# Optimization experiments

Hardware: AMD Instinct MI355X
Metric: run time of the kernel (lower is better)

The kernel has to match this reference:

```python
import jax, jax.numpy as jnp
import numpy as np

HEADS = 8
DIM_HEAD = 64
QUERY_DIM = 1024
CONTEXT_DIM = 768
INNER = HEADS * DIM_HEAD  # 512


def setup_inputs() -> dict:
    key = jax.random.key(0)
    ks = jax.random.split(key, 7)
    B, Sq, Skv = 4, 4096, 1024
    x = jax.random.normal(ks[0], (B, Sq, QUERY_DIM), dtype=jnp.float32)
    context = jax.random.normal(ks[1], (B, Skv, CONTEXT_DIM), dtype=jnp.float32)
    # nn.Linear(in, out) weights stored as [out, in]; we use [in, out] for x @ W
    Wq = jax.random.normal(ks[2], (QUERY_DIM, INNER), dtype=jnp.float32) * (QUERY_DIM ** -0.5)
    Wk = jax.random.normal(ks[3], (CONTEXT_DIM, INNER), dtype=jnp.float32) * (CONTEXT_DIM ** -0.5)
    Wv = jax.random.normal(ks[4], (CONTEXT_DIM, INNER), dtype=jnp.float32) * (CONTEXT_DIM ** -0.5)
    Wo = jax.random.normal(ks[5], (INNER, QUERY_DIM), dtype=jnp.float32) * (INNER ** -0.5)
    bo = jax.random.normal(ks[6], (QUERY_DIM,), dtype=jnp.float32) * 0.01
    return {"x": x, "context": context, "Wq": Wq, "Wk": Wk, "Wv": Wv, "Wo": Wo, "bo": bo}


def reference(x, context, Wq, Wk, Wv, Wo, bo):
    B, Sq, _ = x.shape
    h, d = HEADS, DIM_HEAD
    scale = d ** -0.5
    # project and split heads: [B, S, h*d] -> [B, h, S, d]
    q = (x @ Wq).reshape(B, Sq, h, d).transpose(0, 2, 1, 3)
    k = (context @ Wk).reshape(B, -1, h, d).transpose(0, 2, 1, 3)
    v = (context @ Wv).reshape(B, -1, h, d).transpose(0, 2, 1, 3)
    # the torch chunked loop is exactly full softmax attention (softmax is row-wise)
    scores = jnp.einsum('bhid,bhjd->bhij', q, k) * scale
    attn = jax.nn.softmax(scores, axis=-1)
    out = jnp.einsum('bhij,bhjd->bhid', attn, v)  # [B, h, Sq, d]
    out = out.transpose(0, 2, 1, 3).reshape(B, Sq, h * d)
    return out @ Wo + bo
```

## Files before the change

kernel.cpp:

```cpp
#include <hip/hip_runtime.h>

#define SQ 4096
#define SKV 1024
#define BATCH 4
#define NH 8
#define DH 64
#define QD 1024
#define CD 768
#define INNER 512

typedef _Float16 half8 __attribute__((ext_vector_type(8)));
typedef _Float16 half4v __attribute__((ext_vector_type(4)));
typedef float floatx4 __attribute__((ext_vector_type(4)));
typedef float f32x16 __attribute__((ext_vector_type(16)));
typedef unsigned int uint4v __attribute__((ext_vector_type(4)));

#define MFMA16(a, b, c) __builtin_amdgcn_mfma_f32_16x16x32_f16(a, b, c, 0, 0, 0)
#define MFMA32(a, b, c) __builtin_amdgcn_mfma_f32_32x32x16_f16(a, b, c, 0, 0, 0)

#define PLSWAP(a, b) asm("v_permlane32_swap_b32 %0, %1" : "+v"(a), "+v"(b))

#define GLD16(gptr, lptr)                                                            \
  __builtin_amdgcn_global_load_lds(                                                  \
      (const __attribute__((address_space(1))) unsigned int*)(const void*)(gptr),    \
      (__attribute__((address_space(3))) unsigned int*)(void*)(lptr), 16, 0, 0)

__global__ __launch_bounds__(256) void prep(const float* __restrict__ x,
                                            const float* __restrict__ ctx,
                                            const float* __restrict__ Wq,
                                            const float* __restrict__ Wk,
                                            const float* __restrict__ Wv,
                                            const float* __restrict__ Wo,
                                            _Float16* __restrict__ xh,
                                            _Float16* __restrict__ ctxh,
                                            _Float16* __restrict__ wqt,
                                            _Float16* __restrict__ wkvt,
                                            _Float16* __restrict__ wot) {
  __shared__ float tile[32][33];
  const size_t NX = (size_t)BATCH * SQ * QD;
  const size_t NC = (size_t)BATCH * SKV * CD;
  const unsigned NCAST = (unsigned)((NX + NC) / 2048);

  if (blockIdx.x < NCAST) {
    size_t i = ((size_t)blockIdx.x * 256 + threadIdx.x) * 8;
    const float* s;
    _Float16* d;
    size_t off;
    if (i < NX) { s = x; d = xh; off = i; }
    else        { s = ctx; d = ctxh; off = i - NX; }
    floatx4 a = *(const floatx4*)(s + off);
    floatx4 b = *(const floatx4*)(s + off + 4);
    half8 h;
#pragma unroll
    for (int j = 0; j < 4; ++j) { h[j] = (_Float16)a[j]; h[4 + j] = (_Float16)b[j]; }
    *(half8*)(d + off) = h;
    return;
  }
  const unsigned t = blockIdx.x - NCAST;
  const int z = t >> 10, rem = t & 1023;
  const float* src; _Float16* dst; int R, C;
  if (z == 0)      { src = Wq; dst = wqt;                        R = QD;    C = INNER; }
  else if (z == 1) { src = Wk; dst = wkvt;                       R = CD;    C = INNER; }
  else if (z == 2) { src = Wv; dst = wkvt + (size_t)INNER * CD;  R = CD;    C = INNER; }
  else             { src = Wo; dst = wot;                        R = INNER; C = QD;   }
  const int c0 = (rem & 31) * 32, r0 = (rem >> 5) * 32;
  if (c0 >= C || r0 >= R) return;
  const int tx = threadIdx.x & 31, ty = threadIdx.x >> 5;
#pragma unroll
  for (int i = 0; i < 32; i += 8)
    tile[ty + i][tx] = src[(size_t)(r0 + ty + i) * C + c0 + tx];
  __syncthreads();
#pragma unroll
  for (int i = 0; i < 32; i += 8)
    dst[(size_t)(c0 + ty + i) * R + r0 + tx] = (_Float16)tile[tx][ty + i];
}

template <int MODE>
__device__ __forceinline__ void gemm_body(const _Float16* __restrict__ A,
                                          const _Float16* __restrict__ Bt,
                                          void* __restrict__ Cout,
                                          void* __restrict__ Cout2,
                                          const float* __restrict__ bias,
                                          int M, int N, int K, int bx, int by,
                                          _Float16* As16, _Float16* Bs) {
  const int tid = threadIdx.x;
  const int wave = tid >> 6, lane = tid & 63;
  const int quad = lane >> 4, l16 = lane & 15;
  const int wm = (wave >> 1) * 64, wn = (wave & 1) * 64;
  const size_t n0 = (size_t)bx * 128, m0 = (size_t)by * 128;

  floatx4 acc[4][4] = {};

  const _Float16* ag = A + (m0 + (tid >> 2)) * (size_t)K + (tid & 3) * 8;
  const _Float16* bg = Bt + (n0 + (tid >> 2)) * (size_t)K + (tid & 3) * 8;

#define GSTAGE(bi, k0)                                                      \
  do {                                                                      \
    GLD16(ag + (k0), As16 + (bi)*4096 + tid * 8);                           \
    GLD16(ag + (k0) + (size_t)64 * K, As16 + (bi)*4096 + tid * 8 + 2048);   \
    GLD16(bg + (k0), Bs + (bi)*4096 + tid * 8);                             \
    GLD16(bg + (k0) + (size_t)64 * K, Bs + (bi)*4096 + tid * 8 + 2048);     \
  } while (0)

  const int NT = K / 32;
  GSTAGE(0, 0);
  for (int t = 0; t < NT; ++t) {
    __syncthreads();
    if (t + 1 < NT) GSTAGE((t + 1) & 1, (t + 1) * 32);
    const _Float16* as = As16 + (t & 1) * 4096;
    const _Float16* bs = Bs + (t & 1) * 4096;

    half8 af[4], bf[4];
#pragma unroll
    for (int mt = 0; mt < 4; ++mt)
      af[mt] = *(const half8*)(as + (wm + mt * 16 + l16) * 32 + quad * 8);
#pragma unroll
    for (int nt = 0; nt < 4; ++nt)
      bf[nt] = *(const half8*)(bs + (wn + nt * 16 + l16) * 32 + quad * 8);
    __builtin_amdgcn_s_setprio(1);
#pragma unroll
    for (int mt = 0; mt < 4; ++mt)
#pragma unroll
      for (int nt = 0; nt < 4; ++nt)
        acc[mt][nt] = MFMA16(af[mt], bf[nt], acc[mt][nt]);
    __builtin_amdgcn_s_setprio(0);
  }
#undef GSTAGE

  if (MODE == 3) {
    _Float16* C = (_Float16*)Cout;
    const float sc = 0.125f * 1.44269504088896f;
#pragma unroll
    for (int mt = 0; mt < 4; ++mt) {
      const size_t row = m0 + wm + mt * 16 + quad * 4;
#pragma unroll
      for (int nt = 0; nt < 4; ++nt) {
        const size_t col = n0 + wn + nt * 16 + l16;
#pragma unroll
        for (int r = 0; r < 4; ++r)
          C[(row + r) * N + col] = (_Float16)(acc[mt][nt][r] * sc);
      }
    }
  } else if (MODE == 4) {
    if (n0 < INNER) {
      _Float16* C = (_Float16*)Cout;
#pragma unroll
      for (int mt = 0; mt < 4; ++mt) {
        const size_t row = m0 + wm + mt * 16 + quad * 4;
#pragma unroll
        for (int nt = 0; nt < 4; ++nt) {
          const size_t col = n0 + wn + nt * 16 + l16;
#pragma unroll
          for (int r = 0; r < 4; ++r)
            C[(row + r) * INNER + col] = (_Float16)acc[mt][nt][r];
        }
      }
    } else {
      _Float16* C = (_Float16*)Cout2;
      const int b = (int)(m0 >> 10);
#pragma unroll
      for (int mt = 0; mt < 4; ++mt) {
        const int kvb = (int)(m0 & 1023) + wm + mt * 16 + quad * 4;
#pragma unroll
        for (int nt = 0; nt < 4; ++nt) {
          const int col = (int)(n0 - INNER + wn + nt * 16 + l16);
          const int h = col >> 6, d = col & 63;
          half4v pk;
#pragma unroll
          for (int r = 0; r < 4; ++r) pk[r] = (_Float16)acc[mt][nt][r];
          *(half4v*)(C + (size_t)((b * NH + h) * DH + d) * SKV + kvb) = pk;
        }
      }
    }
  } else {
    float* C = (float*)Cout;
#pragma unroll
    for (int mt = 0; mt < 4; ++mt) {
      const size_t row = m0 + wm + mt * 16 + quad * 4;
#pragma unroll
      for (int nt = 0; nt < 4; ++nt) {
        const size_t col = n0 + wn + nt * 16 + l16;
        const float bb = bias[col];
#pragma unroll
        for (int r = 0; r < 4; ++r)
          C[(row + r) * N + col] = acc[mt][nt][r] + bb;
      }
    }
  }
}

__global__ __launch_bounds__(256) void proj_fused(const _Float16* __restrict__ xh,
                                                  const _Float16* __restrict__ ctxh,
                                                  const _Float16* __restrict__ wqt,
                                                  const _Float16* __restrict__ wkvt,
                                                  _Float16* __restrict__ qh,
                                                  _Float16* __restrict__ kh,
                                                  _Float16* __restrict__ vth) {
  __shared__ _Float16 As16[2 * 128 * 32];
  __shared__ _Float16 Bs[2 * 128 * 32];
  const int b = blockIdx.x;
  const int xcd = b & 7, j = b >> 3;
  const int seg = j % 3;
  if (seg == 2) {
    const int jkv = j / 3;
    gemm_body<4>(ctxh, wkvt, kh, vth, nullptr, BATCH * SKV, 2 * INNER, CD,
                 jkv & 7, xcd * 4 + (jkv >> 3), As16, Bs);
  } else {
    const int jq = (j / 3) * 2 + seg;
    gemm_body<3>(xh, wqt, qh, nullptr, nullptr, BATCH * SQ, INNER, QD,
                 jq & 3, xcd * 16 + (jq >> 2), As16, Bs);
  }
}

__global__ __launch_bounds__(256) void gemm_out(const _Float16* __restrict__ A,
                                                const _Float16* __restrict__ Bt,
                                                float* __restrict__ Cout,
                                                const float* __restrict__ bias) {
  __shared__ _Float16 As16[2 * 128 * 32];
  __shared__ _Float16 Bs[2 * 128 * 32];
  const int b = blockIdx.x;
  const int xcd = b & 7, i = b >> 3;
  gemm_body<2>(A, Bt, Cout, nullptr, bias, BATCH * SQ, QD, INNER,
               i & 7, xcd * 16 + (i >> 3), As16, Bs);
}

__global__ __launch_bounds__(256, 3) void flash_attn8(const _Float16* __restrict__ Q,
                                                      const _Float16* __restrict__ Kp,
                                                      const _Float16* __restrict__ Vt,
                                                      _Float16* __restrict__ O) {
  __shared__ _Float16 Ksb[2 * 64 * 64];
  __shared__ _Float16 Vsb[2 * 64 * 64];
  const int tid = threadIdx.x;
  const int wave = tid >> 6, lane = tid & 63;
  const int l31 = lane & 31, hi = lane >> 5, x7 = lane & 7;

  const int flat = blockIdx.x;
  const int nf = (flat & 7) * 128 + (flat >> 3);
  const int qblk = nf & 31, bh = nf >> 5;
  const int b = bh >> 3, h = bh & 7;

  const size_t qrow0 = (size_t)b * SQ + qblk * 128 + wave * 32;
  const _Float16* qptr = Q + qrow0 * INNER + h * DH;
  const _Float16* kbase = Kp + (size_t)b * SKV * INNER + h * DH;
  const _Float16* vbase = Vt + (size_t)bh * DH * SKV;

  const int kr = tid >> 3;
  const int kb = (tid & 7) ^ (kr & 7);
  const _Float16* kg = kbase + (size_t)kr * INNER + kb * 8;
  const _Float16* vg = vbase + (size_t)kr * SKV + kb * 8;

#define STAGE_KV(bi, tt)                                                        \
  do {                                                                          \
    _Float16* _kl = Ksb + (bi) * 4096 + tid * 8;                                \
    _Float16* _vl = Vsb + (bi) * 4096 + tid * 8;                                \
    GLD16(kg + (size_t)((tt) * 64) * INNER, _kl);                               \
    GLD16(kg + (size_t)((tt) * 64 + 32) * INNER, _kl + 2048);                   \
    GLD16(vg + (tt) * 64, _vl);                                                 \
    GLD16(vg + (size_t)32 * SKV + (tt) * 64, _vl + 2048);                       \
  } while (0)

  half8 aq[4];
#pragma unroll
  for (int i = 0; i < 4; ++i)
    aq[i] = *(const half8*)(qptr + (size_t)l31 * INNER + i * 16 + hi * 8);

  int koff[4], voffB[4];
#pragma unroll
  for (int i = 0; i < 4; ++i)
    koff[i] = l31 * 64 + (((i * 2 + hi) ^ x7) << 3);
#pragma unroll
  for (int j = 0; j < 4; ++j)
    voffB[j] = l31 * 64 + (((j * 2 + hi) ^ x7) << 3);

  half8 ones;
#pragma unroll
  for (int j = 0; j < 8; ++j) ones[j] = (_Float16)1.0f;

  f32x16 o0 = {}, o1 = {}, osum = {};

  STAGE_KV(0, 0);

  for (int t = 0; t < SKV / 64; ++t) {
    __syncthreads();
    if (t < SKV / 64 - 1) STAGE_KV((t + 1) & 1, t + 1);
    const _Float16* ks = Ksb + (t & 1) * 4096;
    const _Float16* vs = Vsb + (t & 1) * 4096;

#pragma unroll
    for (int c2 = 0; c2 < 2; ++c2) {
      half8 ak[4];
#pragma unroll
      for (int i = 0; i < 4; ++i)
        ak[i] = *(const half8*)(ks + c2 * 2048 + koff[i]);

      f32x16 st = {};
#pragma unroll
      for (int i = 0; i < 4; ++i) st = MFMA32(ak[i], aq[i], st);

      unsigned w[8];
#pragma unroll
      for (int j = 0; j < 8; ++j) {
        float plo = __builtin_exp2f(st[2 * j]);
        float phi = __builtin_exp2f(st[2 * j + 1]);
        w[j] = __builtin_bit_cast(unsigned, __builtin_amdgcn_cvt_pkrtz(plo, phi));
      }
      PLSWAP(w[0], w[2]);
      PLSWAP(w[1], w[3]);
      PLSWAP(w[4], w[6]);
      PLSWAP(w[5], w[7]);
      uint4v u0 = {w[0], w[1], w[2], w[3]};
      uint4v u1 = {w[4], w[5], w[6], w[7]};
      half8 A0 = __builtin_bit_cast(half8, u0);
      half8 A1 = __builtin_bit_cast(half8, u1);

      osum = MFMA32(A0, ones, osum);
      osum = MFMA32(A1, ones, osum);

      {
        half8 bv00 = *(const half8*)(vs + 0 * 2048 + voffB[c2 * 2 + 0]);
        half8 bv10 = *(const half8*)(vs + 1 * 2048 + voffB[c2 * 2 + 0]);
        o0 = MFMA32(A0, bv00, o0);
        o1 = MFMA32(A0, bv10, o1);
        half8 bv01 = *(const half8*)(vs + 0 * 2048 + voffB[c2 * 2 + 1]);
        half8 bv11 = *(const half8*)(vs + 1 * 2048 + voffB[c2 * 2 + 1]);
        o0 = MFMA32(A1, bv01, o0);
        o1 = MFMA32(A1, bv11, o1);
      }
    }
  }

  float inv16[16];
#pragma unroll
  for (int r = 0; r < 16; ++r) inv16[r] = 1.0f / osum[r];

  _Float16* op = O + qrow0 * INNER + h * DH;
#pragma unroll
  for (int r = 0; r < 16; ++r) {
    const int q = (r & 3) + 8 * (r >> 2) + 4 * hi;
    op[(size_t)q * INNER + l31] = (_Float16)(o0[r] * inv16[r]);
    op[(size_t)q * INNER + 32 + l31] = (_Float16)(o1[r] * inv16[r]);
  }
#undef STAGE_KV
}

extern "C" void kernel_launch(void* const* d_in, const int* in_sizes, int n_in,
                              void* d_out, int out_size, void* d_ws, size_t ws_size,
                              hipStream_t stream) {
  const float* x   = (const float*)d_in[0];
  const float* ctx = (const float*)d_in[1];
  const float* Wq  = (const float*)d_in[2];
  const float* Wk  = (const float*)d_in[3];
  const float* Wv  = (const float*)d_in[4];
  const float* Wo  = (const float*)d_in[5];
  const float* bo  = (const float*)d_in[6];
  float* out = (float*)d_out;

  const size_t NX = (size_t)BATCH * SQ * QD;
  const size_t NC = (size_t)BATCH * SKV * CD;

  _Float16* ws = (_Float16*)d_ws;
  _Float16* xh   = ws;
  _Float16* ctxh = xh + NX;
  _Float16* wqt  = ctxh + NC;
  _Float16* wkvt = wqt + (size_t)INNER * QD;
  _Float16* wot  = wkvt + (size_t)2 * INNER * CD;
  _Float16* qh   = wot + (size_t)QD * INNER;
  _Float16* kh   = qh + (size_t)BATCH * SQ * INNER;
  _Float16* vth  = kh + (size_t)BATCH * SKV * INNER;
  _Float16* aoh  = xh;

  prep<<<dim3((unsigned)((NX + NC) / 2048) + 4096), 256, 0, stream>>>(
      x, ctx, Wq, Wk, Wv, Wo, xh, ctxh, wqt, wkvt, wot);

  proj_fused<<<dim3(768), 256, 0, stream>>>(xh, ctxh, wqt, wkvt, qh, kh, vth);

  flash_attn8<<<dim3(BATCH * NH * SQ / 128), 256, 0, stream>>>(qh, kh, vth, aoh);

  gemm_out<<<dim3(1024), 256, 0, stream>>>(aoh, wot, out, bo);
}
```

Measured before the change: 262.4 us.

## Fuse fp32-to-fp16 activation cast into projection GEMM loads

Removes the separate cast pass that converted x and context to fp16 in a workspace. The projection GEMM now streams fp32 activations straight into LDS and converts them to fp16 while building MFMA fragments. This saves one full write and re-read of the activations, but it doubles the A-tile LDS footprint and the global bytes per tile in the GEMM, and adds conversion instructions to the inner loop. The weight transpose kernel now uses a 3D grid.

```diff
diff --git a/kernel.cpp b/kernel.cpp
--- a/kernel.cpp
+++ b/kernel.cpp
@@ -25,45 +25,21 @@
       (const __attribute__((address_space(1))) unsigned int*)(const void*)(gptr),    \
       (__attribute__((address_space(3))) unsigned int*)(void*)(lptr), 16, 0, 0)
 
-__global__ __launch_bounds__(256) void prep(const float* __restrict__ x,
-                                            const float* __restrict__ ctx,
-                                            const float* __restrict__ Wq,
-                                            const float* __restrict__ Wk,
-                                            const float* __restrict__ Wv,
-                                            const float* __restrict__ Wo,
-                                            _Float16* __restrict__ xh,
-                                            _Float16* __restrict__ ctxh,
-                                            _Float16* __restrict__ wqt,
-                                            _Float16* __restrict__ wkvt,
-                                            _Float16* __restrict__ wot) {
+__global__ __launch_bounds__(256) void transpose_all(const float* __restrict__ Wq,
+                                                     const float* __restrict__ Wk,
+                                                     const float* __restrict__ Wv,
+                                                     const float* __restrict__ Wo,
+                                                     _Float16* __restrict__ wqt,
+                                                     _Float16* __restrict__ wkvt,
+                                                     _Float16* __restrict__ wot) {
   __shared__ float tile[32][33];
-  const size_t NX = (size_t)BATCH * SQ * QD;
-  const size_t NC = (size_t)BATCH * SKV * CD;
-  const unsigned NCAST = (unsigned)((NX + NC) / 2048);
-
-  if (blockIdx.x < NCAST) {
-    size_t i = ((size_t)blockIdx.x * 256 + threadIdx.x) * 8;
-    const float* s;
-    _Float16* d;
-    size_t off;
-    if (i < NX) { s = x; d = xh; off = i; }
-    else        { s = ctx; d = ctxh; off = i - NX; }
-    floatx4 a = *(const floatx4*)(s + off);
-    floatx4 b = *(const floatx4*)(s + off + 4);
-    half8 h;
-#pragma unroll
-    for (int j = 0; j < 4; ++j) { h[j] = (_Float16)a[j]; h[4 + j] = (_Float16)b[j]; }
-    *(half8*)(d + off) = h;
-    return;
-  }
-  const unsigned t = blockIdx.x - NCAST;
-  const int z = t >> 10, rem = t & 1023;
+  const int z = blockIdx.z;
   const float* src; _Float16* dst; int R, C;
   if (z == 0)      { src = Wq; dst = wqt;                        R = QD;    C = INNER; }
   else if (z == 1) { src = Wk; dst = wkvt;                       R = CD;    C = INNER; }
   else if (z == 2) { src = Wv; dst = wkvt + (size_t)INNER * CD;  R = CD;    C = INNER; }
   else             { src = Wo; dst = wot;                        R = INNER; C = QD;   }
-  const int c0 = (rem & 31) * 32, r0 = (rem >> 5) * 32;
+  const int c0 = blockIdx.x * 32, r0 = blockIdx.y * 32;
   if (c0 >= C || r0 >= R) return;
   const int tx = threadIdx.x & 31, ty = threadIdx.x >> 5;
 #pragma unroll
@@ -75,14 +51,16 @@
     dst[(size_t)(c0 + ty + i) * R + r0 + tx] = (_Float16)tile[tx][ty + i];
 }
 
-template <int MODE>
-__device__ __forceinline__ void gemm_body(const _Float16* __restrict__ A,
+template <int MODE, int AF32>
+__device__ __forceinline__ void gemm_body(const void* __restrict__ Aany,
                                           const _Float16* __restrict__ Bt,
                                           void* __restrict__ Cout,
                                           void* __restrict__ Cout2,
                                           const float* __restrict__ bias,
                                           int M, int N, int K, int bx, int by,
-                                          _Float16* As16, _Float16* Bs) {
+                                          void* AsRaw, _Float16* Bs) {
+  float* As32 = (float*)AsRaw;
+  _Float16* As16 = (_Float16*)AsRaw;
   const int tid = threadIdx.x;
   const int wave = tid >> 6, lane = tid & 63;
   const int quad = lane >> 4, l16 = lane & 15;
@@ -91,15 +69,23 @@
 
   floatx4 acc[4][4] = {};
 
-  const _Float16* ag = A + (m0 + (tid >> 2)) * (size_t)K + (tid & 3) * 8;
+  const float* a32g = (const float*)Aany + (m0 + (tid >> 3)) * (size_t)K + (tid & 7) * 4;
+  const _Float16* a16g = (const _Float16*)Aany + (m0 + (tid >> 2)) * (size_t)K + (tid & 3) * 8;
   const _Float16* bg = Bt + (n0 + (tid >> 2)) * (size_t)K + (tid & 3) * 8;
 
-#define GSTAGE(bi, k0)                                                      \
-  do {                                                                      \
-    GLD16(ag + (k0), As16 + (bi)*4096 + tid * 8);                           \
-    GLD16(ag + (k0) + (size_t)64 * K, As16 + (bi)*4096 + tid * 8 + 2048);   \
-    GLD16(bg + (k0), Bs + (bi)*4096 + tid * 8);                             \
-    GLD16(bg + (k0) + (size_t)64 * K, Bs + (bi)*4096 + tid * 8 + 2048);     \
+#define GSTAGE(bi, k0)                                                        \
+  do {                                                                        \
+    if (AF32) {                                                               \
+      GLD16(a32g + (k0), As32 + (bi)*4096 + tid * 4);                         \
+      GLD16(a32g + (k0) + (size_t)32 * K, As32 + (bi)*4096 + tid * 4 + 1024); \
+      GLD16(a32g + (k0) + (size_t)64 * K, As32 + (bi)*4096 + tid * 4 + 2048); \
+      GLD16(a32g + (k0) + (size_t)96 * K, As32 + (bi)*4096 + tid * 4 + 3072); \
+    } else {                                                                  \
+      GLD16(a16g + (k0), As16 + (bi)*4096 + tid * 8);                         \
+      GLD16(a16g + (k0) + (size_t)64 * K, As16 + (bi)*4096 + tid * 8 + 2048); \
+    }                                                                         \
+    GLD16(bg + (k0), Bs + (bi)*4096 + tid * 8);                               \
+    GLD16(bg + (k0) + (size_t)64 * K, Bs + (bi)*4096 + tid * 8 + 2048);       \
   } while (0)
 
   const int NT = K / 32;
@@ -107,16 +93,26 @@
   for (int t = 0; t < NT; ++t) {
     __syncthreads();
     if (t + 1 < NT) GSTAGE((t + 1) & 1, (t + 1) * 32);
-    const _Float16* as = As16 + (t & 1) * 4096;
-    const _Float16* bs = Bs + (t & 1) * 4096;
+    const int bo = (t & 1) * 4096;
 
     half8 af[4], bf[4];
 #pragma unroll
-    for (int mt = 0; mt < 4; ++mt)
-      af[mt] = *(const half8*)(as + (wm + mt * 16 + l16) * 32 + quad * 8);
+    for (int mt = 0; mt < 4; ++mt) {
+      const int row = wm + mt * 16 + l16;
+      if (AF32) {
+        floatx4 x0 = *(const floatx4*)(As32 + bo + row * 32 + quad * 8);
+        floatx4 x1 = *(const floatx4*)(As32 + bo + row * 32 + quad * 8 + 4);
+        half8 tt;
+#pragma unroll
+        for (int i = 0; i < 4; ++i) { tt[i] = (_Float16)x0[i]; tt[4 + i] = (_Float16)x1[i]; }
+        af[mt] = tt;
+      } else {
+        af[mt] = *(const half8*)(As16 + bo + row * 32 + quad * 8);
+      }
+    }
 #pragma unroll
     for (int nt = 0; nt < 4; ++nt)
-      bf[nt] = *(const half8*)(bs + (wn + nt * 16 + l16) * 32 + quad * 8);
+      bf[nt] = *(const half8*)(Bs + bo + (wn + nt * 16 + l16) * 32 + quad * 8);
     __builtin_amdgcn_s_setprio(1);
 #pragma unroll
     for (int mt = 0; mt < 4; ++mt)
@@ -189,26 +185,26 @@
   }
 }
 
-__global__ __launch_bounds__(256) void proj_fused(const _Float16* __restrict__ xh,
-                                                  const _Float16* __restrict__ ctxh,
+__global__ __launch_bounds__(256) void proj_fused(const float* __restrict__ x,
+                                                  const float* __restrict__ ctx,
                                                   const _Float16* __restrict__ wqt,
                                                   const _Float16* __restrict__ wkvt,
                                                   _Float16* __restrict__ qh,
                                                   _Float16* __restrict__ kh,
                                                   _Float16* __restrict__ vth) {
-  __shared__ _Float16 As16[2 * 128 * 32];
+  __shared__ float As32[2 * 128 * 32];
   __shared__ _Float16 Bs[2 * 128 * 32];
   const int b = blockIdx.x;
   const int xcd = b & 7, j = b >> 3;
   const int seg = j % 3;
   if (seg == 2) {
     const int jkv = j / 3;
-    gemm_body<4>(ctxh, wkvt, kh, vth, nullptr, BATCH * SKV, 2 * INNER, CD,
-                 jkv & 7, xcd * 4 + (jkv >> 3), As16, Bs);
+    gemm_body<4, 1>((const void*)ctx, wkvt, kh, vth, nullptr, BATCH * SKV,
+                    2 * INNER, CD, jkv & 7, xcd * 4 + (jkv >> 3), As32, Bs);
   } else {
     const int jq = (j / 3) * 2 + seg;
-    gemm_body<3>(xh, wqt, qh, nullptr, nullptr, BATCH * SQ, INNER, QD,
-                 jq & 3, xcd * 16 + (jq >> 2), As16, Bs);
+    gemm_body<3, 1>((const void*)x, wqt, qh, nullptr, nullptr, BATCH * SQ,
+                    INNER, QD, jq & 3, xcd * 16 + (jq >> 2), As32, Bs);
   }
 }
 
@@ -220,8 +216,8 @@
   __shared__ _Float16 Bs[2 * 128 * 32];
   const int b = blockIdx.x;
   const int xcd = b & 7, i = b >> 3;
-  gemm_body<2>(A, Bt, Cout, nullptr, bias, BATCH * SQ, QD, INNER,
-               i & 7, xcd * 16 + (i >> 3), As16, Bs);
+  gemm_body<2, 0>((const void*)A, Bt, Cout, nullptr, bias, BATCH * SQ, QD, INNER,
+                  i & 7, xcd * 16 + (i >> 3), As16, Bs);
 }
 
 __global__ __launch_bounds__(256, 3) void flash_attn8(const _Float16* __restrict__ Q,
@@ -355,24 +351,18 @@
   const float* bo  = (const float*)d_in[6];
   float* out = (float*)d_out;
 
-  const size_t NX = (size_t)BATCH * SQ * QD;
-  const size_t NC = (size_t)BATCH * SKV * CD;
-
   _Float16* ws = (_Float16*)d_ws;
-  _Float16* xh   = ws;
-  _Float16* ctxh = xh + NX;
-  _Float16* wqt  = ctxh + NC;
+  _Float16* wqt  = ws;
   _Float16* wkvt = wqt + (size_t)INNER * QD;
   _Float16* wot  = wkvt + (size_t)2 * INNER * CD;
   _Float16* qh   = wot + (size_t)QD * INNER;
   _Float16* kh   = qh + (size_t)BATCH * SQ * INNER;
   _Float16* vth  = kh + (size_t)BATCH * SKV * INNER;
-  _Float16* aoh  = xh;
-
-  prep<<<dim3((unsigned)((NX + NC) / 2048) + 4096), 256, 0, stream>>>(
-      x, ctx, Wq, Wk, Wv, Wo, xh, ctxh, wqt, wkvt, wot);
-
-  proj_fused<<<dim3(768), 256, 0, stream>>>(xh, ctxh, wqt, wkvt, qh, kh, vth);
+  _Float16* aoh  = vth + (size_t)BATCH * SKV * INNER;
+
+  transpose_all<<<dim3(32, 32, 4), 256, 0, stream>>>(Wq, Wk, Wv, Wo, wqt, wkvt, wot);
+
+  proj_fused<<<dim3(768), 256, 0, stream>>>(x, ctx, wqt, wkvt, qh, kh, vth);
 
   flash_attn8<<<dim3(BATCH * NH * SQ / 128), 256, 0, stream>>>(qh, kh, vth, aoh);
 
```

Result: faster. 255.6 us (-2.6%).

## Triple-buffer GEMM LDS staging with vmcnt waits and XOR-swizzled layout

Applied to the files above, without the earlier changes.

The shared GEMM body moves from a double-buffered LDS pipeline to a three-stage ring. It prefetches two tiles ahead and waits on vmcnt counts instead of a full sync before each stage, so global loads overlap more with MFMA work. The global-to-LDS load column is also XOR-swizzled by row, and the fragment reads use the matching swizzle to reduce LDS bank conflicts. This costs 50% more LDS per block for the projection and output GEMMs, which may lower occupancy, and it relies on getting the hand-written wait counts right.

```diff
diff --git a/kernel.cpp b/kernel.cpp
--- a/kernel.cpp
+++ b/kernel.cpp
@@ -91,8 +91,9 @@
 
   floatx4 acc[4][4] = {};
 
-  const _Float16* ag = A + (m0 + (tid >> 2)) * (size_t)K + (tid & 3) * 8;
-  const _Float16* bg = Bt + (n0 + (tid >> 2)) * (size_t)K + (tid & 3) * 8;
+  const int a16r = tid >> 2, a16b = (tid & 3) ^ ((a16r >> 1) & 3);
+  const _Float16* ag = A + (m0 + a16r) * (size_t)K + a16b * 8;
+  const _Float16* bg = Bt + (n0 + a16r) * (size_t)K + a16b * 8;
 
 #define GSTAGE(bi, k0)                                                      \
   do {                                                                      \
@@ -104,19 +105,31 @@
 
   const int NT = K / 32;
   GSTAGE(0, 0);
+  GSTAGE(1, 32);
+  int cb = 0;
   for (int t = 0; t < NT; ++t) {
-    __syncthreads();
-    if (t + 1 < NT) GSTAGE((t + 1) & 1, (t + 1) * 32);
-    const _Float16* as = As16 + (t & 1) * 4096;
-    const _Float16* bs = Bs + (t & 1) * 4096;
-
+    if (t + 1 < NT)
+      asm volatile("s_waitcnt vmcnt(4)" ::: "memory");
+    else
+      asm volatile("s_waitcnt vmcnt(0)" ::: "memory");
+    __builtin_amdgcn_sched_barrier(0);
+    __builtin_amdgcn_s_barrier();
+    __builtin_amdgcn_sched_barrier(0);
+    if (t + 2 < NT) {
+      int nb = cb + 2; if (nb >= 3) nb -= 3;
+      GSTAGE(nb, (t + 2) * 32);
+    }
+    const _Float16* as = As16 + cb * 4096;
+    const _Float16* bs = Bs + cb * 4096;
+
+    const int r2 = (l16 >> 1) & 3;
     half8 af[4], bf[4];
 #pragma unroll
     for (int mt = 0; mt < 4; ++mt)
-      af[mt] = *(const half8*)(as + (wm + mt * 16 + l16) * 32 + quad * 8);
+      af[mt] = *(const half8*)(as + (wm + mt * 16 + l16) * 32 + (quad ^ r2) * 8);
 #pragma unroll
     for (int nt = 0; nt < 4; ++nt)
-      bf[nt] = *(const half8*)(bs + (wn + nt * 16 + l16) * 32 + quad * 8);
+      bf[nt] = *(const half8*)(bs + (wn + nt * 16 + l16) * 32 + (quad ^ r2) * 8);
     __builtin_amdgcn_s_setprio(1);
 #pragma unroll
     for (int mt = 0; mt < 4; ++mt)
@@ -124,6 +137,7 @@
       for (int nt = 0; nt < 4; ++nt)
         acc[mt][nt] = MFMA16(af[mt], bf[nt], acc[mt][nt]);
     __builtin_amdgcn_s_setprio(0);
+    cb = (cb == 2) ? 0 : cb + 1;
   }
 #undef GSTAGE
 
@@ -196,8 +210,8 @@
                                                   _Float16* __restrict__ qh,
                                                   _Float16* __restrict__ kh,
                                                   _Float16* __restrict__ vth) {
-  __shared__ _Float16 As16[2 * 128 * 32];
-  __shared__ _Float16 Bs[2 * 128 * 32];
+  __shared__ _Float16 As16[3 * 128 * 32];
+  __shared__ _Float16 Bs[3 * 128 * 32];
   const int b = blockIdx.x;
   const int xcd = b & 7, j = b >> 3;
   const int seg = j % 3;
@@ -216,8 +230,8 @@
                                                 const _Float16* __restrict__ Bt,
                                                 float* __restrict__ Cout,
                                                 const float* __restrict__ bias) {
-  __shared__ _Float16 As16[2 * 128 * 32];
-  __shared__ _Float16 Bs[2 * 128 * 32];
+  __shared__ _Float16 As16[3 * 128 * 32];
+  __shared__ _Float16 Bs[3 * 128 * 32];
   const int b = blockIdx.x;
   const int xcd = b & 7, i = b >> 3;
   gemm_body<2>(A, Bt, Cout, nullptr, bias, BATCH * SQ, QD, INNER,
```

Result: no change. 257.8 us (-1.8%).
